# Performance work log

Measured on AMD Instinct MI355X. Metric: run time of the kernel, lower is better.

Reference implementation:

```python
import jax, jax.numpy as jnp
import numpy as np

B, F, T, D = 64, 128, 64, 256  # batch, n_features, time_length, temporalDim


def setup_inputs() -> dict:
    key = jax.random.key(0)
    ks = jax.random.split(key, 7)
    return {
        "x": jax.random.normal(ks[0], (B, F, T), dtype=jnp.float32),
        # Conv1d(1, D, 1) per timestep: weight [D,1,1] and bias [D] stacked over T -> [T, D]
        "wconv": jax.random.normal(ks[1], (T, D), dtype=jnp.float32) * 0.1,
        "bconv": jax.random.normal(ks[2], (T, D), dtype=jnp.float32) * 0.1,
        # W1: ParameterList of [D,1] -> [T, D]; b1: list of [1,F] -> [T, F]
        "w1": jax.random.normal(ks[3], (T, D), dtype=jnp.float32),
        "b1": jax.random.normal(ks[4], (T, F), dtype=jnp.float32),
        # W2: [D,1] -> [D]; b2: [1,T] -> [T]
        "w2": jax.random.normal(ks[5], (D,), dtype=jnp.float32),
        "b2": jax.random.normal(ks[6], (T,), dtype=jnp.float32),
    }


def reference(x, wconv, bconv, w1, b1, w2, b2):
    # Dropout is identity (eval mode).
    # Kernel-size-1 Conv1d over [B,1,F] == outer product of the scalar x[b,f,t] with wconv[t] + bias.
    xt = jnp.transpose(x, (0, 2, 1))                      # [B, T, F]
    sT = xt[..., None] * wconv[None, :, None, :] + bconv[None, :, None, :]  # [B, T, F, D]
    # per-step variable attention: sigmoid(sT @ W1 + b1)
    vatt = jax.nn.sigmoid(jnp.einsum("btfd,td->btf", sT, w1) + b1[None])    # [B, T, F]
    # attention-pooled per-step representation
    result = jnp.einsum("btf,btfd->btd", vatt, sT)        # [B, T, D]
    # temporal attention over steps
    tatt = jax.nn.sigmoid(jnp.einsum("btd,d->bt", result, w2) + b2[None])   # [B, T]
    out = jnp.einsum("bt,btd->bd", tatt, result)          # [B, D]
    variAtten = jnp.transpose(vatt, (0, 2, 1))            # [B, F, T]
    return out, variAtten * tatt[:, None, :]
```

## Files before the change

kernel.cpp:

```cpp
#include <hip/hip_runtime.h>
#include <math.h>

#define B 64
#define F 128
#define T 64
#define D 256
#define TC 16
#define NC (T / TC)

__global__ __launch_bounds__(256) void fused_kernel(
    const float* __restrict__ x,
    const float* __restrict__ wconv, const float* __restrict__ bconv,
    const float* __restrict__ w1, const float* __restrict__ b1,
    const float* __restrict__ w2, const float* __restrict__ b2,
    float* __restrict__ out1, float* __restrict__ out2) {

    __shared__ float b1_s[F * (TC + 1)];
    __shared__ float A_s[TC], C_s[TC], P_s[TC], Q_s[TC];
    __shared__ float s0red[4 * TC], s1red[4 * TC];
    __shared__ float s0_s[TC], s1_s[TC], tatt_s[TC];

    const int blk = blockIdx.x;
    const int b  = blk & (B - 1);
    const int c  = blk >> 6;
    const int t0 = c * TC;
    const int tid  = threadIdx.x;
    const int w    = tid >> 6;
    const int lane = tid & 63;
    const int fg   = tid >> 4;
    const int lt   = tid & (TC - 1);

    const float* xb = x + b * F * T + t0 + lt;
    float xv[8];
    #pragma unroll
    for (int i = 0; i < 8; ++i) xv[i] = xb[(fg + 16 * i) * T];

    #pragma unroll
    for (int k = 0; k < (TC * F) / 256; ++k) {
        const int lin = tid + 256 * k;
        const int tl  = lin >> 7;
        const int f   = lin & (F - 1);
        b1_s[f * (TC + 1) + tl] = b1[(t0 + tl) * F + f];
    }

    {
        const float4 w2v = *reinterpret_cast<const float4*>(w2 + lane * 4);
        #pragma unroll
        for (int j = 0; j < 4; ++j) {
            const int tl = w * 4 + j;
            const int base = (t0 + tl) * D + lane * 4;
            const float4 wc  = *reinterpret_cast<const float4*>(wconv + base);
            const float4 bc  = *reinterpret_cast<const float4*>(bconv + base);
            const float4 w1v = *reinterpret_cast<const float4*>(w1 + base);
            float a  = wc.x*w1v.x + wc.y*w1v.y + wc.z*w1v.z + wc.w*w1v.w;
            float cc = bc.x*w1v.x + bc.y*w1v.y + bc.z*w1v.z + bc.w*w1v.w;
            float p  = wc.x*w2v.x + wc.y*w2v.y + wc.z*w2v.z + wc.w*w2v.w;
            float q  = bc.x*w2v.x + bc.y*w2v.y + bc.z*w2v.z + bc.w*w2v.w;
            #pragma unroll
            for (int off = 32; off > 0; off >>= 1) {
                a  += __shfl_down(a, off);
                cc += __shfl_down(cc, off);
                p  += __shfl_down(p, off);
                q  += __shfl_down(q, off);
            }
            if (lane == 0) { A_s[tl] = a; C_s[tl] = cc; P_s[tl] = p; Q_s[tl] = q; }
        }
    }
    __syncthreads();

    const float At = A_s[lt], Ct = C_s[lt];
    float vreg[8];
    float s0 = 0.f, s1 = 0.f;
    #pragma unroll
    for (int i = 0; i < 8; ++i) {
        const int f = fg + 16 * i;
        const float z = xv[i] * At + Ct + b1_s[f * (TC + 1) + lt];
        const float v = 1.0f / (1.0f + __expf(-z));
        vreg[i] = v;
        s0 += v;
        s1 += v * xv[i];
    }
    s0 += __shfl_down(s0, 32); s1 += __shfl_down(s1, 32);
    s0 += __shfl_down(s0, 16); s1 += __shfl_down(s1, 16);
    if (lane < TC) { s0red[w * TC + lane] = s0; s1red[w * TC + lane] = s1; }
    __syncthreads();

    if (tid < TC) {
        const float S0 = s0red[tid] + s0red[TC + tid] + s0red[2*TC + tid] + s0red[3*TC + tid];
        const float S1 = s1red[tid] + s1red[TC + tid] + s1red[2*TC + tid] + s1red[3*TC + tid];
        const float z  = S1 * P_s[tid] + S0 * Q_s[tid] + b2[t0 + tid];
        s0_s[tid] = S0;
        s1_s[tid] = S1;
        tatt_s[tid] = 1.0f / (1.0f + __expf(-z));
    }
    __syncthreads();

    float acc = 0.f;
    #pragma unroll
    for (int j = 0; j < TC; ++j) {
        const int t = t0 + j;
        acc += tatt_s[j] * (wconv[t * D + tid] * s1_s[j] + bconv[t * D + tid] * s0_s[j]);
    }
    atomicAdd(out1 + b * D + tid, acc);

    float* o2 = out2 + b * F * T + t0 + lt;
    const float ta = tatt_s[lt];
    #pragma unroll
    for (int i = 0; i < 8; ++i) {
        o2[(fg + 16 * i) * T] = vreg[i] * ta;
    }
}

extern "C" void kernel_launch(void* const* d_in, const int* in_sizes, int n_in,
                              void* d_out, int out_size, void* d_ws, size_t ws_size,
                              hipStream_t stream) {
    const float* x     = (const float*)d_in[0];
    const float* wconv = (const float*)d_in[1];
    const float* bconv = (const float*)d_in[2];
    const float* w1    = (const float*)d_in[3];
    const float* b1    = (const float*)d_in[4];
    const float* w2    = (const float*)d_in[5];
    const float* b2    = (const float*)d_in[6];
    float* out = (float*)d_out;

    hipMemsetAsync(out, 0, B * D * sizeof(float), stream);
    fused_kernel<<<B * NC, 256, 0, stream>>>(x, wconv, bconv, w1, b1, w2, b2,
                                             out, out + B * D);
}
```

Measured before the change: 71.32 us.

## Use one 1024-thread block per batch to drop memset and atomics

Each batch element is now handled by a single 1024-thread block covering all 64 timesteps instead of four 256-thread blocks over 16-step chunks. out1 is reduced inside the block through shared memory and written directly, which removes the hipMemsetAsync launch and the global atomicAdds. vatt is staged in shared memory so out2 is written with coalesced row-major stores. The cost is a 64-block grid that occupies few CUs, about 90KB of LDS per block, and each block redoing the weight dot products for all 64 timesteps.

```diff
diff --git a/kernel.cpp b/kernel.cpp
--- a/kernel.cpp
+++ b/kernel.cpp
@@ -5,50 +5,46 @@
 #define F 128
 #define T 64
 #define D 256
-#define TC 16
-#define NC (T / TC)
 
-__global__ __launch_bounds__(256) void fused_kernel(
+__global__ __launch_bounds__(1024) void fused_kernel(
     const float* __restrict__ x,
     const float* __restrict__ wconv, const float* __restrict__ bconv,
     const float* __restrict__ w1, const float* __restrict__ b1,
     const float* __restrict__ w2, const float* __restrict__ b2,
     float* __restrict__ out1, float* __restrict__ out2) {
 
-    __shared__ float b1_s[F * (TC + 1)];
-    __shared__ float A_s[TC], C_s[TC], P_s[TC], Q_s[TC];
-    __shared__ float s0red[4 * TC], s1red[4 * TC];
-    __shared__ float s0_s[TC], s1_s[TC], tatt_s[TC];
+    __shared__ float vatt_s[F * T];
+    __shared__ float b1_s[F * (T + 1)];
+    __shared__ float s0red[16 * T], s1red[16 * T];
+    __shared__ float part1[4 * D];
+    __shared__ float A_s[T], C_s[T], P_s[T], Q_s[T];
+    __shared__ float s0_s[T], s1_s[T], tatt_s[T];
 
-    const int blk = blockIdx.x;
-    const int b  = blk & (B - 1);
-    const int c  = blk >> 6;
-    const int t0 = c * TC;
+    const int b    = blockIdx.x;
     const int tid  = threadIdx.x;
     const int w    = tid >> 6;
     const int lane = tid & 63;
-    const int fg   = tid >> 4;
-    const int lt   = tid & (TC - 1);
 
-    const float* xb = x + b * F * T + t0 + lt;
+    const float* xb = x + b * F * T;
+
     float xv[8];
     #pragma unroll
-    for (int i = 0; i < 8; ++i) xv[i] = xb[(fg + 16 * i) * T];
+    for (int i = 0; i < 8; ++i) xv[i] = xb[(w + 16 * i) * T + lane];
 
     #pragma unroll
-    for (int k = 0; k < (TC * F) / 256; ++k) {
-        const int lin = tid + 256 * k;
-        const int tl  = lin >> 7;
-        const int f   = lin & (F - 1);
-        b1_s[f * (TC + 1) + tl] = b1[(t0 + tl) * F + f];
+    for (int k = 0; k < (T * F) / 1024; ++k) {
+        const int lin = tid + 1024 * k;
+        const int t = lin >> 7;
+        const int f = lin & (F - 1);
+        b1_s[f * (T + 1) + t] = b1[lin];
     }
 
     {
         const float4 w2v = *reinterpret_cast<const float4*>(w2 + lane * 4);
         #pragma unroll
         for (int j = 0; j < 4; ++j) {
-            const int tl = w * 4 + j;
-            const int base = (t0 + tl) * D + lane * 4;
+            const int t = w * 4 + j;
+            const int base = t * D + lane * 4;
             const float4 wc  = *reinterpret_cast<const float4*>(wconv + base);
             const float4 bc  = *reinterpret_cast<const float4*>(bconv + base);
             const float4 w1v = *reinterpret_cast<const float4*>(w1 + base);
@@ -63,51 +59,62 @@
                 p  += __shfl_down(p, off);
                 q  += __shfl_down(q, off);
             }
-            if (lane == 0) { A_s[tl] = a; C_s[tl] = cc; P_s[tl] = p; Q_s[tl] = q; }
+            if (lane == 0) { A_s[t] = a; C_s[t] = cc; P_s[t] = p; Q_s[t] = q; }
         }
     }
     __syncthreads();
 
-    const float At = A_s[lt], Ct = C_s[lt];
-    float vreg[8];
+    const float At = A_s[lane], Ct = C_s[lane];
     float s0 = 0.f, s1 = 0.f;
     #pragma unroll
     for (int i = 0; i < 8; ++i) {
-        const int f = fg + 16 * i;
-        const float z = xv[i] * At + Ct + b1_s[f * (TC + 1) + lt];
+        const int f = w + 16 * i;
+        const float z = xv[i] * At + Ct + b1_s[f * (T + 1) + lane];
         const float v = 1.0f / (1.0f + __expf(-z));
-        vreg[i] = v;
+        vatt_s[f * T + lane] = v;
         s0 += v;
         s1 += v * xv[i];
     }
-    s0 += __shfl_down(s0, 32); s1 += __shfl_down(s1, 32);
-    s0 += __shfl_down(s0, 16); s1 += __shfl_down(s1, 16);
-    if (lane < TC) { s0red[w * TC + lane] = s0; s1red[w * TC + lane] = s1; }
+    s0red[w * T + lane] = s0;
+    s1red[w * T + lane] = s1;
     __syncthreads();
 
-    if (tid < TC) {
-        const float S0 = s0red[tid] + s0red[TC + tid] + s0red[2*TC + tid] + s0red[3*TC + tid];
-        const float S1 = s1red[tid] + s1red[TC + tid] + s1red[2*TC + tid] + s1red[3*TC + tid];
-        const float z  = S1 * P_s[tid] + S0 * Q_s[tid] + b2[t0 + tid];
+    if (tid < T) {
+        float S0 = 0.f, S1 = 0.f;
+        #pragma unroll
+        for (int ww = 0; ww < 16; ++ww) {
+            S0 += s0red[ww * T + tid];
+            S1 += s1red[ww * T + tid];
+        }
+        const float z = S1 * P_s[tid] + S0 * Q_s[tid] + b2[tid];
         s0_s[tid] = S0;
         s1_s[tid] = S1;
         tatt_s[tid] = 1.0f / (1.0f + __expf(-z));
     }
     __syncthreads();
 
-    float acc = 0.f;
+    {
+        const int wg = tid >> 8;
+        const int d  = tid & (D - 1);
+        float acc = 0.f;
+        #pragma unroll
+        for (int j = 0; j < 16; ++j) {
+            const int t = wg * 16 + j;
+            acc += tatt_s[t] * (wconv[t * D + d] * s1_s[t] + bconv[t * D + d] * s0_s[t]);
+        }
+        part1[wg * D + d] = acc;
+    }
+
+    float* o2 = out2 + b * F * T;
     #pragma unroll
-    for (int j = 0; j < TC; ++j) {
-        const int t = t0 + j;
-        acc += tatt_s[j] * (wconv[t * D + tid] * s1_s[j] + bconv[t * D + tid] * s0_s[j]);
+    for (int k = 0; k < (F * T) / 1024; ++k) {
+        const int lin = tid + 1024 * k;
+        o2[lin] = vatt_s[lin] * tatt_s[lin & (T - 1)];
     }
-    atomicAdd(out1 + b * D + tid, acc);
+    __syncthreads();
 
-    float* o2 = out2 + b * F * T + t0 + lt;
-    const float ta = tatt_s[lt];
-    #pragma unroll
-    for (int i = 0; i < 8; ++i) {
-        o2[(fg + 16 * i) * T] = vreg[i] * ta;
+    if (tid < D) {
+        out1[b * D + tid] = part1[tid] + part1[D + tid] + part1[2 * D + tid] + part1[3 * D + tid];
     }
 }
 
@@ -123,7 +130,6 @@
     const float* b2    = (const float*)d_in[6];
     float* out = (float*)d_out;
 
-    hipMemsetAsync(out, 0, B * D * sizeof(float), stream);
-    fused_kernel<<<B * NC, 256, 0, stream>>>(x, wconv, bconv, w1, b1, w2, b2,
-                                             out, out + B * D);
+    fused_kernel<<<B, 1024, 0, stream>>>(x, wconv, bconv, w1, b1, w2, b2,
+                                         out, out + B * D);
 }
```

New measurement: 73.33 us. 1.03x slower.
